# Performance work log

Measured on AMD Instinct MI355X. Metric: run time of the kernel, lower is better.

## Reference

```python
import jax, jax.numpy as jnp
import numpy as np

B, N, D_MODEL, H = 2, 2048, 1024, 16
Q_CHUNK, K_CHUNK = 512, 1024
LN_EPS = 1e-5


def layer_norm(x, g, b):
    mu = x.mean(-1, keepdims=True)
    var = ((x - mu) ** 2).mean(-1, keepdims=True)
    return (x - mu) * jax.lax.rsqrt(var + LN_EPS) * g + b


def chunked_attention(q, k, v, qry_chunk, key_chunk):
    # q,k,v: [b,h,n,d]; memory-efficient chunked online-softmax attention
    b, h, n, d = q.shape
    q = q * (d ** -0.5)
    Q, K = n // qry_chunk, n // key_chunk
    qr = q.reshape(b, h, Q, qry_chunk, d)
    kr = k.reshape(b, h, K, key_chunk, d)
    vr = v.reshape(b, h, K, key_chunk, d)
    # per (q-chunk, k-chunk) scores: [b,h,Q,K,i,j]
    qk = jnp.einsum('bhqid,bhkjd->bhqkij', qr, kr)
    qk_max = jax.lax.stop_gradient(qk.max(axis=-1, keepdims=True))  # [b,h,Q,K,i,1]
    exp_qk = jnp.exp(qk - qk_max)
    attn = jnp.einsum('bhqkij,bhkjd->bhqkid', exp_qk, vr)
    exp_sum = exp_qk.sum(-1)            # [b,h,Q,K,i]
    m = qk_max[..., 0]                  # [b,h,Q,K,i]
    gmax = m.max(axis=3, keepdims=True)  # global max over key chunks
    renorm = jax.lax.stop_gradient(jnp.exp(m - gmax))
    num = (attn * renorm[..., None]).sum(axis=3)       # [b,h,Q,i,d]
    den = (exp_sum * renorm).sum(axis=3)[..., None]    # [b,h,Q,i,1]
    out = num / (1e-8 + den)
    return out.reshape(b, h, n, d)


def setup_inputs() -> dict:
    key = jax.random.key(0)
    ks = jax.random.split(key, 10)
    s = 0.02
    return {
        'x': jax.random.normal(ks[0], (B, N, D_MODEL), dtype=jnp.float32),
        'Wq': jax.random.normal(ks[1], (D_MODEL, D_MODEL), dtype=jnp.float32) * s,
        'bq': jnp.zeros((D_MODEL,), jnp.float32),
        'Wk': jax.random.normal(ks[2], (D_MODEL, D_MODEL), dtype=jnp.float32) * s,
        'bk': jnp.zeros((D_MODEL,), jnp.float32),
        'Wv': jax.random.normal(ks[3], (D_MODEL, D_MODEL), dtype=jnp.float32) * s,
        'bv': jnp.zeros((D_MODEL,), jnp.float32),
        'Wo': jax.random.normal(ks[4], (D_MODEL, D_MODEL), dtype=jnp.float32) * s,
        'bo': jnp.zeros((D_MODEL,), jnp.float32),
        'ln_g': jnp.ones((D_MODEL,), jnp.float32),
        'ln_b': jnp.zeros((D_MODEL,), jnp.float32),
    }


def reference(x, Wq, bq, Wk, bk, Wv, bv, Wo, bo, ln_g, ln_b):
    # qkv adapter: self-attention (key = val = qry = x)
    q = x @ Wq + bq
    k = x @ Wk + bk
    v = x @ Wv + bv
    # pre-norm on query path
    q = layer_norm(q, ln_g, ln_b)
    b, n, _ = q.shape
    d = D_MODEL // H
    qh = q.reshape(b, n, H, d).transpose(0, 2, 1, 3)
    kh = k.reshape(b, n, H, d).transpose(0, 2, 1, 3)
    vh = v.reshape(b, n, H, d).transpose(0, 2, 1, 3)
    attn = chunked_attention(qh, kh, vh, Q_CHUNK, K_CHUNK)
    out = attn.transpose(0, 2, 1, 3).reshape(b, n, D_MODEL)
    out = out + q  # residual with normed projected query
    return out @ Wo + bo
```

## Files before the change

kernel.cpp:

```cpp
#include <hip/hip_runtime.h>


typedef unsigned short u16;
typedef __attribute__((ext_vector_type(8))) short bf8v;
typedef __attribute__((ext_vector_type(4))) float f4v;

typedef __attribute__((address_space(1))) void gvoid;
typedef __attribute__((address_space(3))) void lvoid;
__device__ __forceinline__ void cp16(const void* g, void* l) {
  __builtin_amdgcn_global_load_lds((gvoid*)g, (lvoid*)l, 16, 0, 0);
}

__device__ __forceinline__ float bf2f(u16 u) {
  unsigned int x = ((unsigned int)u) << 16;
  float f; __builtin_memcpy(&f, &x, 4); return f;
}
__device__ __forceinline__ u16 f2bf(float f) {
  unsigned int x; __builtin_memcpy(&x, &f, 4);
  unsigned int r = (x + 0x7fffu + ((x >> 16) & 1u)) >> 16;
  return (u16)r;
}
__device__ __forceinline__ unsigned pack2bf(float a, float b) {
  unsigned ua, ub;
  __builtin_memcpy(&ua, &a, 4); __builtin_memcpy(&ub, &b, 4);
  return __builtin_amdgcn_perm(ub, ua, 0x07060302u);
}

#define KSCALE 0.18033688011f

__global__ void k_classify(const u16* a0, const u16* a1, const u16* a2, const u16* a3,
                           const u16* a4, const u16* a5, const u16* a6, const u16* a7,
                           const u16* a8, const u16* a9, const u16* a10, int* flags) {
  int t = threadIdx.x;
  if (t >= 11) return;
  const u16* arr[11] = {a0,a1,a2,a3,a4,a5,a6,a7,a8,a9,a10};
  const u16* p = arr[t];
  int ze = 0, no = 0, pe = 0;
  for (int i = 0; i < 128; ++i) {
    u16 he = p[2*i], ho = p[2*i+1];
    if (he == 0) ze++;
    if (ho != 0) no++;
    int e = (he >> 7) & 0xff;
    if (he == 0 || (e >= 64 && e <= 160)) pe++;
  }
  int isbf;
  if (ze >= 100 && no >= 64) isbf = 0;
  else isbf = (pe >= 100) ? 1 : 0;
  flags[t] = isbf;
}

__global__ __launch_bounds__(256) void k_convert_x(const void* xin, u16* xb, const int* flags) {
  size_t i = ((size_t)blockIdx.x * 256 + threadIdx.x) * 8;
  if (flags[0]) {
    *(float4*)(xb + i) = *((const float4*)((const u16*)xin + i));
  } else {
    const float* xf = (const float*)xin;
    float4 a = *(const float4*)(xf + i);
    float4 b = *(const float4*)(xf + i + 4);
    ushort4 o0, o1;
    o0.x = f2bf(a.x); o0.y = f2bf(a.y); o0.z = f2bf(a.z); o0.w = f2bf(a.w);
    o1.x = f2bf(b.x); o1.y = f2bf(b.y); o1.z = f2bf(b.z); o1.w = f2bf(b.w);
    *(ushort4*)(xb + i) = o0; *(ushort4*)(xb + i + 4) = o1;
  }
}

__global__ __launch_bounds__(256) void k_transpose_w(const void* W0, const void* W1,
    const void* W2, const void* W3, u16* wt, const int* flags) {
  __shared__ u16 tile[64 * 65];
  int z = blockIdx.z;
  const void* W = (z == 0) ? W0 : (z == 1) ? W1 : (z == 2) ? W2 : W3;
  int isb = flags[1 + 2*z];
  u16* dst = wt + (size_t)z * (1u << 20);
  int r0 = blockIdx.y * 64, c0 = blockIdx.x * 64;
  int t = threadIdx.x;
  for (int rr = 0; rr < 2; ++rr) {
    int row = rr * 32 + (t >> 3);
    int c8 = (t & 7) * 8;
    u16 v[8];
    if (isb) {
      const u16* Ws = (const u16*)W;
      ushort4 a = *(const ushort4*)&Ws[(size_t)(r0 + row) * 1024 + c0 + c8];
      ushort4 b = *(const ushort4*)&Ws[(size_t)(r0 + row) * 1024 + c0 + c8 + 4];
      v[0]=a.x; v[1]=a.y; v[2]=a.z; v[3]=a.w; v[4]=b.x; v[5]=b.y; v[6]=b.z; v[7]=b.w;
    } else {
      const float* Wf = (const float*)W;
      float4 a = *(const float4*)&Wf[(size_t)(r0 + row) * 1024 + c0 + c8];
      float4 b = *(const float4*)&Wf[(size_t)(r0 + row) * 1024 + c0 + c8 + 4];
      v[0]=f2bf(a.x); v[1]=f2bf(a.y); v[2]=f2bf(a.z); v[3]=f2bf(a.w);
      v[4]=f2bf(b.x); v[5]=f2bf(b.y); v[6]=f2bf(b.z); v[7]=f2bf(b.w);
    }
#pragma unroll
    for (int j = 0; j < 8; ++j) tile[row * 65 + c8 + j] = v[j];
  }
  __syncthreads();
  for (int rr = 0; rr < 2; ++rr) {
    int nrow = rr * 32 + (t >> 3);
    int k8 = (t & 7) * 8;
    u16 v[8];
#pragma unroll
    for (int j = 0; j < 8; ++j) v[j] = tile[(k8 + j) * 65 + nrow];
    ushort4 o0, o1;
    o0.x=v[0]; o0.y=v[1]; o0.z=v[2]; o0.w=v[3];
    o1.x=v[4]; o1.y=v[5]; o1.z=v[6]; o1.w=v[7];
    *(ushort4*)&dst[(size_t)(c0 + nrow) * 1024 + r0 + k8] = o0;
    *(ushort4*)&dst[(size_t)(c0 + nrow) * 1024 + r0 + k8 + 4] = o1;
  }
}

template <int MT>
__device__ __forceinline__ void gemm_bt(const u16* __restrict__ A, const u16* __restrict__ Bt,
    const void* __restrict__ bias, int bias_bf, void* __restrict__ Cout, int mode,
    float cscale) {
  constexpr int MI = MT / 32;
  __shared__ __align__(16) u16 As[2][MT * 32];
  __shared__ __align__(16) u16 Bs[2][128 * 32];
  const int tid = threadIdx.x;
  const int wave = tid >> 6, lane = tid & 63;
  const int qd = lane >> 4, ln = lane & 15;
  const int m0 = blockIdx.y * MT, n0 = blockIdx.x * 128;
  const int wr = (wave >> 1) * (MT / 2), wc = (wave & 1) * 64;
  const int r0 = wave * 16 + (lane >> 2);
  const int csrc = ((lane & 3) ^ ((lane >> 2) & 3)) * 8;
  const u16* Ag = &A[(size_t)m0 * 1024];
  const u16* Bg = &Bt[(size_t)n0 * 1024];
  const int co = (qd ^ (ln & 3)) * 8;
  f4v acc[MI][4];
#pragma unroll
  for (int i = 0; i < MI; ++i)
#pragma unroll
    for (int j = 0; j < 4; ++j) acc[i][j] = (f4v){0.f, 0.f, 0.f, 0.f};

#pragma unroll
  for (int t = 0; t < MT / 64; ++t)
    cp16(&Ag[(size_t)(t * 64 + r0) * 1024 + csrc], &As[0][(t * 256 + wave * 64) * 8]);
#pragma unroll
  for (int t = 0; t < 2; ++t)
    cp16(&Bg[(size_t)(t * 64 + r0) * 1024 + csrc], &Bs[0][(t * 256 + wave * 64) * 8]);

  for (int it = 0; it < 32; ++it) {
    __syncthreads();
    if (it < 31) {
      int ko = (it + 1) * 32;
      int bi = (it + 1) & 1;
#pragma unroll
      for (int t = 0; t < MT / 64; ++t)
        cp16(&Ag[(size_t)(t * 64 + r0) * 1024 + ko + csrc], &As[bi][(t * 256 + wave * 64) * 8]);
#pragma unroll
      for (int t = 0; t < 2; ++t)
        cp16(&Bg[(size_t)(t * 64 + r0) * 1024 + ko + csrc], &Bs[bi][(t * 256 + wave * 64) * 8]);
    }
    const u16* as = As[it & 1];
    const u16* bs = Bs[it & 1];
    bf8v af[MI], bfr[4];
#pragma unroll
    for (int i = 0; i < MI; ++i) af[i]  = *(const bf8v*)&as[(wr + i * 16 + ln) * 32 + co];
#pragma unroll
    for (int j = 0; j < 4; ++j) bfr[j] = *(const bf8v*)&bs[(wc + j * 16 + ln) * 32 + co];
#pragma unroll
    for (int i = 0; i < MI; ++i)
#pragma unroll
      for (int j = 0; j < 4; ++j)
        acc[i][j] = __builtin_amdgcn_mfma_f32_16x16x32_bf16(af[i], bfr[j], acc[i][j], 0, 0, 0);
  }
#pragma unroll
  for (int j = 0; j < 4; ++j) {
    int col = n0 + wc + j * 16 + ln;
    float bv = bias_bf ? bf2f(((const u16*)bias)[col]) : ((const float*)bias)[col];
#pragma unroll
    for (int i = 0; i < MI; ++i) {
      int row = m0 + wr + i * 16 + qd * 4;
      if (mode == 2) {
        ushort4 o4;
        o4.x = f2bf((acc[i][j][0] + bv) * cscale);
        o4.y = f2bf((acc[i][j][1] + bv) * cscale);
        o4.z = f2bf((acc[i][j][2] + bv) * cscale);
        o4.w = f2bf((acc[i][j][3] + bv) * cscale);
        int l = row & 63;
        int pos = (((l >> 5) << 2 | ((l >> 2) & 3)) << 3) | ((l & 16) >> 2);
        int n = row & 2047;
        size_t vidx = ((size_t)((row >> 11) * 16 + (col >> 6))) * (64 * 2048)
                    + (size_t)(col & 63) * 2048 + (n & ~63) + pos;
        *(ushort4*)&((u16*)Cout)[vidx] = o4;
      } else {
#pragma unroll
        for (int r = 0; r < 4; ++r) {
          float v = (acc[i][j][r] + bv) * cscale;
          if (mode == 1) ((u16*)Cout)[(size_t)(row + r) * 1024 + col] = f2bf(v);
          else           ((float*)Cout)[(size_t)(row + r) * 1024 + col] = v;
        }
      }
    }
  }
}

__global__ __launch_bounds__(256) void k_gemm_qkv(const u16* xb, const u16* wt,
    const void* bq, const void* bk, const void* bv, const int* flags,
    u16* qpre, u16* kb, u16* vtb) {
  int z = blockIdx.z;
  const u16* Bt = wt + (size_t)z * (1u << 20);
  const void* bias = (z == 0) ? bq : (z == 1) ? bk : bv;
  if (z == 0)      gemm_bt<128>(xb, Bt, bias, flags[2], qpre, 1, 1.0f);
  else if (z == 1) gemm_bt<128>(xb, Bt, bias, flags[4], kb,   1, KSCALE);
  else             gemm_bt<128>(xb, Bt, bias, flags[6], vtb,  2, 1.0f);
}

__global__ __launch_bounds__(256) void k_gemm_out(const u16* A, const u16* Bt,
    const void* bias, const int* flags, void* out) {
  gemm_bt<64>(A, Bt, bias, flags[8], out, flags[0] ? 1 : 0, 1.0f);
}

__global__ __launch_bounds__(256) void k_layernorm(const u16* __restrict__ qp,
    const void* __restrict__ g, const void* __restrict__ bb, const int* flags,
    u16* __restrict__ out) {
  int row = blockIdx.x, t = threadIdx.x;
  const u16* rp = qp + (size_t)row * 1024;
  ushort4 u = *(const ushort4*)(rp + t * 4);
  float x0 = bf2f(u.x), x1 = bf2f(u.y), x2 = bf2f(u.z), x3 = bf2f(u.w);
  float s = x0 + x1 + x2 + x3;
  float s2 = x0 * x0 + x1 * x1 + x2 * x2 + x3 * x3;
  for (int off = 32; off; off >>= 1) { s += __shfl_down(s, off); s2 += __shfl_down(s2, off); }
  __shared__ float red[10];
  int wave = t >> 6, lane = t & 63;
  if (lane == 0) { red[wave] = s; red[4 + wave] = s2; }
  __syncthreads();
  if (t == 0) {
    float S = red[0] + red[1] + red[2] + red[3];
    float S2 = red[4] + red[5] + red[6] + red[7];
    float mu = S * (1.f / 1024.f);
    float var = S2 * (1.f / 1024.f) - mu * mu;
    red[8] = mu; red[9] = rsqrtf(var + 1e-5f);
  }
  __syncthreads();
  float mu = red[8], rstd = red[9];
  int gf = flags[9], bf = flags[10];
  int c = t * 4;
  float gv[4], bv[4];
#pragma unroll
  for (int k = 0; k < 4; ++k) {
    gv[k] = gf ? bf2f(((const u16*)g)[c + k]) : ((const float*)g)[c + k];
    bv[k] = bf ? bf2f(((const u16*)bb)[c + k]) : ((const float*)bb)[c + k];
  }
  ushort4 o;
  o.x = f2bf((x0 - mu) * rstd * gv[0] + bv[0]);
  o.y = f2bf((x1 - mu) * rstd * gv[1] + bv[1]);
  o.z = f2bf((x2 - mu) * rstd * gv[2] + bv[2]);
  o.w = f2bf((x3 - mu) * rstd * gv[3] + bv[3]);
  *(ushort4*)(out + (size_t)row * 1024 + c) = o;
}

__global__ __launch_bounds__(128, 2) void k_attention(const u16* __restrict__ qln,
    const u16* __restrict__ kb, const u16* __restrict__ vt, u16* __restrict__ attn) {
  const int qt = blockIdx.x, h = blockIdx.y, b = blockIdx.z;
  const int tid = threadIdx.x, wave = tid >> 6, lane = tid & 63;
  const int qd = lane >> 4, ln = lane & 15;
  __shared__ __align__(16) u16 Ks[2][64 * 64];
  __shared__ __align__(16) u16 Vs[2][64 * 64];
  const int qrow0 = qt * 64 + wave * 32;

  const u16* kgb = kb + (size_t)b * 2048 * 1024 + h * 64;
  const u16* vgb = vt + ((size_t)(b * 16 + h)) * 64 * 2048;

  bf8v qf[2][2];
#pragma unroll
  for (int qs = 0; qs < 2; ++qs) {
    const u16* qb = qln + ((size_t)b * 2048 + qrow0 + qs * 16 + ln) * 1024 + h * 64;
    qf[qs][0] = *(const bf8v*)(qb + qd * 8);
    qf[qs][1] = *(const bf8v*)(qb + 32 + qd * 8);
  }
  float ls[2][4];
  f4v o[2][4];
#pragma unroll
  for (int qs = 0; qs < 2; ++qs)
#pragma unroll
    for (int r = 0; r < 4; ++r) { ls[qs][r] = 0.f; o[qs][r] = (f4v){0.f, 0.f, 0.f, 0.f}; }

  const int swz  = (qd ^ (ln & 7)) * 8;
  const int swz4 = ((qd + 4) ^ (ln & 7)) * 8;
  const int lr8 = lane >> 3;
  const int cs8 = lane & 7;

#define STAGE(kt, bi)                                                          \
  {                                                                            \
    _Pragma("unroll")                                                          \
    for (int t = 0; t < 4; ++t) {                                              \
      int row = wave * 32 + t * 8 + lr8;                                       \
      int cs = (cs8 ^ (row & 7)) * 8;                                          \
      cp16(&kgb[(size_t)((kt) + row) * 1024 + cs], &Ks[bi][(wave * 32 + t * 8) * 64]); \
      cp16(&vgb[(size_t)row * 2048 + (kt) + cs],   &Vs[bi][(wave * 32 + t * 8) * 64]); \
    }                                                                          \
  }

  STAGE(0, 0);
  for (int it = 0; it < 32; ++it) {
    __syncthreads();
    if (it < 31) STAGE((it + 1) * 64, (it + 1) & 1);
    const u16* K = Ks[it & 1];
    const u16* V = Vs[it & 1];

    bf8v kf[4][2];
#pragma unroll
    for (int ct = 0; ct < 4; ++ct) {
      kf[ct][0] = *(const bf8v*)&K[(ct * 16 + ln) * 64 + swz];
      kf[ct][1] = *(const bf8v*)&K[(ct * 16 + ln) * 64 + swz4];
    }
    unsigned pk[2][4][2];
#pragma unroll
    for (int qs = 0; qs < 2; ++qs) {
#pragma unroll
      for (int ct = 0; ct < 4; ++ct) {
        f4v z = (f4v){0.f, 0.f, 0.f, 0.f};
        z = __builtin_amdgcn_mfma_f32_16x16x32_bf16(kf[ct][0], qf[qs][0], z, 0, 0, 0);
        z = __builtin_amdgcn_mfma_f32_16x16x32_bf16(kf[ct][1], qf[qs][1], z, 0, 0, 0);
        float p0 = __builtin_amdgcn_exp2f(z[0]);
        float p1 = __builtin_amdgcn_exp2f(z[1]);
        float p2 = __builtin_amdgcn_exp2f(z[2]);
        float p3 = __builtin_amdgcn_exp2f(z[3]);
        ls[qs][0] += p0; ls[qs][1] += p1; ls[qs][2] += p2; ls[qs][3] += p3;
        pk[qs][ct][0] = pack2bf(p0, p1);
        pk[qs][ct][1] = pack2bf(p2, p3);
      }
    }
#pragma unroll
    for (int c = 0; c < 2; ++c) {
#pragma unroll
      for (int dt = 0; dt < 4; ++dt) {
        int vrow = dt * 16 + ln;
        bf8v vf = *(const bf8v*)&V[vrow * 64 + (((c * 4 + qd) ^ (vrow & 7)) * 8)];
#pragma unroll
        for (int qs = 0; qs < 2; ++qs) {
          unsigned avals[4] = {pk[qs][2*c][0], pk[qs][2*c][1], pk[qs][2*c+1][0], pk[qs][2*c+1][1]};
          bf8v af; __builtin_memcpy(&af, avals, 16);
          o[qs][dt] = __builtin_amdgcn_mfma_f32_16x16x32_bf16(af, vf, o[qs][dt], 0, 0, 0);
        }
      }
    }
  }
#pragma unroll
  for (int qs = 0; qs < 2; ++qs) {
    float lsum = (ls[qs][0] + ls[qs][1]) + (ls[qs][2] + ls[qs][3]);
    lsum += __shfl_xor(lsum, 16);
    lsum += __shfl_xor(lsum, 32);
    float rden[4];
#pragma unroll
    for (int r = 0; r < 4; ++r) {
      float dv = __shfl(lsum, (lane & 48) + qd * 4 + r);
      rden[r] = __builtin_amdgcn_rcpf(1e-8f + dv);
    }
#pragma unroll
    for (int dt = 0; dt < 4; ++dt) {
#pragma unroll
      for (int r = 0; r < 4; ++r) {
        size_t idx = ((size_t)b * 2048 + qrow0 + qs * 16 + qd * 4 + r) * 1024
                   + h * 64 + dt * 16 + ln;
        float val = o[qs][dt][r] * rden[r] + bf2f(qln[idx]);
        attn[idx] = f2bf(val);
      }
    }
  }
}

extern "C" void kernel_launch(void* const* d_in, const int* in_sizes, int n_in,
                              void* d_out, int out_size, void* d_ws, size_t ws_size,
                              hipStream_t stream) {
  int* flags = (int*)d_ws;
  u16* base = (u16*)((char*)d_ws + 256);
  const size_t M1 = 1u << 20;
  u16* xb   = base;
  u16* wt   = base + 4 * M1;
  u16* qpre = base + 8 * M1;
  u16* kb   = base + 12 * M1;
  u16* vtb  = base + 16 * M1;
  u16* qln = xb;
  u16* at  = qpre;

  k_classify<<<1, 64, 0, stream>>>(
      (const u16*)d_in[0], (const u16*)d_in[1], (const u16*)d_in[2], (const u16*)d_in[3],
      (const u16*)d_in[4], (const u16*)d_in[5], (const u16*)d_in[6], (const u16*)d_in[7],
      (const u16*)d_in[8], (const u16*)d_in[9], (const u16*)d_in[10], flags);

  k_convert_x<<<2048, 256, 0, stream>>>(d_in[0], xb, flags);
  k_transpose_w<<<dim3(16, 16, 4), 256, 0, stream>>>(d_in[1], d_in[3], d_in[5], d_in[7], wt, flags);
  k_gemm_qkv<<<dim3(8, 32, 3), 256, 0, stream>>>(xb, wt, d_in[2], d_in[4], d_in[6], flags,
                                                 qpre, kb, vtb);
  k_layernorm<<<4096, 256, 0, stream>>>(qpre, d_in[9], d_in[10], flags, qln);
  k_attention<<<dim3(32, 16, 2), 128, 0, stream>>>(qln, kb, vtb, at);
  k_gemm_out<<<dim3(8, 64), 256, 0, stream>>>(at, wt + 3 * M1, d_in[8], flags, d_out);
}
```

Before: 231.4 us.

## Pre-layout V in MFMA fragment order and drop LDS staging in attention

The QKV GEMM now writes V directly in per-lane MFMA fragment order, so the attention kernel can load V fragments with contiguous 16-byte global loads. The attention kernel drops shared-memory double buffering and barriers. It uses one wave per block handling 64 query rows, reads K straight from global memory, and remaps block IDs so each XCD serves the same (b,h) heads for L2 locality. This removes LDS traffic and syncs. The cost is uncached per-wave global loads with no prefetch overlap, plus more registers per wave for four query slices.

New measurement: 229.5 us. About the same (-0.8%).

```diff
diff --git a/kernel.cpp b/kernel.cpp
--- a/kernel.cpp
+++ b/kernel.cpp
@@ -175,12 +175,14 @@
         o4.y = f2bf((acc[i][j][1] + bv) * cscale);
         o4.z = f2bf((acc[i][j][2] + bv) * cscale);
         o4.w = f2bf((acc[i][j][3] + bv) * cscale);
-        int l = row & 63;
-        int pos = (((l >> 5) << 2 | ((l >> 2) & 3)) << 3) | ((l & 16) >> 2);
-        int n = row & 2047;
-        size_t vidx = ((size_t)((row >> 11) * 16 + (col >> 6))) * (64 * 2048)
-                    + (size_t)(col & 63) * 2048 + (n & ~63) + pos;
-        *(ushort4*)&((u16*)Cout)[vidx] = o4;
+        int b_ = row >> 11, nl = row & 2047;
+        int h_ = col >> 6, d6 = col & 63;
+        int kt = nl >> 6, b0 = nl & 63;
+        int c = b0 >> 5, g = (b0 >> 4) & 1, qd_f = (b0 >> 2) & 3;
+        int dt = d6 >> 4, ln_f = d6 & 15;
+        size_t off = (size_t)(b_ * 16 + h_) * 131072
+                   + (size_t)(kt * 4096 + (c * 4 + dt) * 512 + (qd_f * 16 + ln_f) * 8 + g * 4);
+        *(ushort4*)&((u16*)Cout)[off] = o4;
       } else {
 #pragma unroll
         for (int r = 0; r < 4; ++r) {
@@ -248,64 +250,50 @@
   *(ushort4*)(out + (size_t)row * 1024 + c) = o;
 }
 
-__global__ __launch_bounds__(128, 2) void k_attention(const u16* __restrict__ qln,
-    const u16* __restrict__ kb, const u16* __restrict__ vt, u16* __restrict__ attn) {
-  const int qt = blockIdx.x, h = blockIdx.y, b = blockIdx.z;
-  const int tid = threadIdx.x, wave = tid >> 6, lane = tid & 63;
+__global__ __launch_bounds__(64) void k_attention(const u16* __restrict__ qln,
+    const u16* __restrict__ kb, const u16* __restrict__ vfg, u16* __restrict__ attn) {
+  const int x = blockIdx.x;
+  const int xcd = x & 7, sl = x >> 3;
+  const int bh = xcd * 4 + (sl >> 5), qt = sl & 31;
+  const int b = bh >> 4, h = bh & 15;
+  const int lane = threadIdx.x;
   const int qd = lane >> 4, ln = lane & 15;
-  __shared__ __align__(16) u16 Ks[2][64 * 64];
-  __shared__ __align__(16) u16 Vs[2][64 * 64];
-  const int qrow0 = qt * 64 + wave * 32;
+  const int qrow0 = qt * 64;
 
   const u16* kgb = kb + (size_t)b * 2048 * 1024 + h * 64;
-  const u16* vgb = vt + ((size_t)(b * 16 + h)) * 64 * 2048;
-
-  bf8v qf[2][2];
-#pragma unroll
-  for (int qs = 0; qs < 2; ++qs) {
+  const u16* vgb = vfg + (size_t)bh * 131072;
+
+  bf8v qf[4][2];
+#pragma unroll
+  for (int qs = 0; qs < 4; ++qs) {
     const u16* qb = qln + ((size_t)b * 2048 + qrow0 + qs * 16 + ln) * 1024 + h * 64;
     qf[qs][0] = *(const bf8v*)(qb + qd * 8);
     qf[qs][1] = *(const bf8v*)(qb + 32 + qd * 8);
   }
-  float ls[2][4];
-  f4v o[2][4];
-#pragma unroll
-  for (int qs = 0; qs < 2; ++qs)
+  float ls[4][4];
+  f4v o[4][4];
+#pragma unroll
+  for (int qs = 0; qs < 4; ++qs)
 #pragma unroll
     for (int r = 0; r < 4; ++r) { ls[qs][r] = 0.f; o[qs][r] = (f4v){0.f, 0.f, 0.f, 0.f}; }
 
-  const int swz  = (qd ^ (ln & 7)) * 8;
-  const int swz4 = ((qd + 4) ^ (ln & 7)) * 8;
-  const int lr8 = lane >> 3;
-  const int cs8 = lane & 7;
-
-#define STAGE(kt, bi)                                                          \
-  {                                                                            \
-    _Pragma("unroll")                                                          \
-    for (int t = 0; t < 4; ++t) {                                              \
-      int row = wave * 32 + t * 8 + lr8;                                       \
-      int cs = (cs8 ^ (row & 7)) * 8;                                          \
-      cp16(&kgb[(size_t)((kt) + row) * 1024 + cs], &Ks[bi][(wave * 32 + t * 8) * 64]); \
-      cp16(&vgb[(size_t)row * 2048 + (kt) + cs],   &Vs[bi][(wave * 32 + t * 8) * 64]); \
-    }                                                                          \
-  }
-
-  STAGE(0, 0);
-  for (int it = 0; it < 32; ++it) {
-    __syncthreads();
-    if (it < 31) STAGE((it + 1) * 64, (it + 1) & 1);
-    const u16* K = Ks[it & 1];
-    const u16* V = Vs[it & 1];
-
+  for (int kt = 0; kt < 2048; kt += 64) {
+    const u16* kr = kgb + (size_t)kt * 1024;
     bf8v kf[4][2];
 #pragma unroll
     for (int ct = 0; ct < 4; ++ct) {
-      kf[ct][0] = *(const bf8v*)&K[(ct * 16 + ln) * 64 + swz];
-      kf[ct][1] = *(const bf8v*)&K[(ct * 16 + ln) * 64 + swz4];
-    }
-    unsigned pk[2][4][2];
-#pragma unroll
-    for (int qs = 0; qs < 2; ++qs) {
+      kf[ct][0] = *(const bf8v*)(kr + (size_t)(ct * 16 + ln) * 1024 + qd * 8);
+      kf[ct][1] = *(const bf8v*)(kr + (size_t)(ct * 16 + ln) * 1024 + 32 + qd * 8);
+    }
+    const u16* vr = vgb + (size_t)(kt >> 6) * 4096;
+    bf8v vf[8];
+#pragma unroll
+    for (int cd = 0; cd < 8; ++cd)
+      vf[cd] = *(const bf8v*)(vr + cd * 512 + lane * 8);
+
+#pragma unroll
+    for (int qs = 0; qs < 4; ++qs) {
+      unsigned pk[4][2];
 #pragma unroll
       for (int ct = 0; ct < 4; ++ct) {
         f4v z = (f4v){0.f, 0.f, 0.f, 0.f};
@@ -316,27 +304,21 @@
         float p2 = __builtin_amdgcn_exp2f(z[2]);
         float p3 = __builtin_amdgcn_exp2f(z[3]);
         ls[qs][0] += p0; ls[qs][1] += p1; ls[qs][2] += p2; ls[qs][3] += p3;
-        pk[qs][ct][0] = pack2bf(p0, p1);
-        pk[qs][ct][1] = pack2bf(p2, p3);
+        pk[ct][0] = pack2bf(p0, p1);
+        pk[ct][1] = pack2bf(p2, p3);
       }
-    }
-#pragma unroll
-    for (int c = 0; c < 2; ++c) {
-#pragma unroll
-      for (int dt = 0; dt < 4; ++dt) {
-        int vrow = dt * 16 + ln;
-        bf8v vf = *(const bf8v*)&V[vrow * 64 + (((c * 4 + qd) ^ (vrow & 7)) * 8)];
-#pragma unroll
-        for (int qs = 0; qs < 2; ++qs) {
-          unsigned avals[4] = {pk[qs][2*c][0], pk[qs][2*c][1], pk[qs][2*c+1][0], pk[qs][2*c+1][1]};
-          bf8v af; __builtin_memcpy(&af, avals, 16);
-          o[qs][dt] = __builtin_amdgcn_mfma_f32_16x16x32_bf16(af, vf, o[qs][dt], 0, 0, 0);
-        }
+#pragma unroll
+      for (int c = 0; c < 2; ++c) {
+        unsigned avals[4] = {pk[2*c][0], pk[2*c][1], pk[2*c+1][0], pk[2*c+1][1]};
+        bf8v af; __builtin_memcpy(&af, avals, 16);
+#pragma unroll
+        for (int dt = 0; dt < 4; ++dt)
+          o[qs][dt] = __builtin_amdgcn_mfma_f32_16x16x32_bf16(af, vf[c * 4 + dt], o[qs][dt], 0, 0, 0);
       }
     }
   }
 #pragma unroll
-  for (int qs = 0; qs < 2; ++qs) {
+  for (int qs = 0; qs < 4; ++qs) {
     float lsum = (ls[qs][0] + ls[qs][1]) + (ls[qs][2] + ls[qs][3]);
     lsum += __shfl_xor(lsum, 16);
     lsum += __shfl_xor(lsum, 32);
@@ -383,6 +365,6 @@
   k_gemm_qkv<<<dim3(8, 32, 3), 256, 0, stream>>>(xb, wt, d_in[2], d_in[4], d_in[6], flags,
                                                  qpre, kb, vtb);
   k_layernorm<<<4096, 256, 0, stream>>>(qpre, d_in[9], d_in[10], flags, qln);
-  k_attention<<<dim3(32, 16, 2), 128, 0, stream>>>(qln, kb, vtb, at);
+  k_attention<<<1024, 64, 0, stream>>>(qln, kb, vtb, at);
   k_gemm_out<<<dim3(8, 64), 256, 0, stream>>>(at, wt + 3 * M1, d_in[8], flags, d_out);
 }
```
